# Kernel tuning notes

Hardware: AMD Instinct MI355X
Metric: run time of the kernel (lower is better)

Reference implementation:

```python
import math
import jax
import jax.numpy as jnp
import numpy as np

B = 4096        # number of contexts / segments
T = 262144      # total objects across all segments (avg 64 per segment)
F = 128         # object_size
H = 256         # hidden_size
C = 512         # context_size


def setup_inputs() -> dict:
    key = jax.random.key(0)
    ks = jax.random.split(key, 8)
    objects = jax.random.normal(ks[0], (T, F), dtype=jnp.float32)
    context = jax.random.normal(ks[1], (B, C), dtype=jnp.float32)
    # sorted segment ids; guarantee every segment non-empty by seeding one id per segment
    extra = jax.random.randint(ks[2], (T - B,), 0, B)
    segment_ids = jnp.sort(jnp.concatenate([jnp.arange(B, dtype=extra.dtype), extra])).astype(jnp.int32)
    s = 0.05
    return {
        "objects": objects,
        "context": context,
        "segment_ids": segment_ids,
        "W1": jax.random.normal(ks[3], (F, H), dtype=jnp.float32) * s,
        "b1": jnp.zeros((H,), dtype=jnp.float32),
        "W2": jax.random.normal(ks[4], (H, H), dtype=jnp.float32) * s,
        "b2": jnp.zeros((H,), dtype=jnp.float32),
        "W3": jax.random.normal(ks[5], (H, 2 * H), dtype=jnp.float32) * s,
        "b3": jnp.zeros((2 * H,), dtype=jnp.float32),
        "Wq": jax.random.normal(ks[6], (C, H), dtype=jnp.float32) * s,
        "bq": jnp.zeros((H,), dtype=jnp.float32),
    }


def reference(objects, context, segment_ids, W1, b1, W2, b2, W3, b3, Wq, bq):
    num_segments = context.shape[0]
    # kv MLP: Linear -> ReLU -> Linear -> ReLU -> Linear(2H)
    h = jax.nn.relu(objects @ W1 + b1)
    h = jax.nn.relu(h @ W2 + b2)
    kv = h @ W3 + b3                                   # [T, 2H]
    k, v = jnp.split(kv, 2, axis=1)                    # [T, H] each
    # query per object via repeat_interleave == gather by segment id
    q = (context @ Wq + bq)[segment_ids]               # [T, H]
    logits = jnp.sum(q * k, axis=1) / math.sqrt(k.shape[1])   # [T]
    # per-segment stable softmax
    m = jax.ops.segment_max(logits, segment_ids, num_segments=num_segments)
    e = jnp.exp(logits - m[segment_ids])
    z = jax.ops.segment_sum(e, segment_ids, num_segments=num_segments)
    w = e / z[segment_ids]                             # [T]
    # per-segment weighted sum of values
    embedding = jax.ops.segment_sum(w[:, None] * v, segment_ids, num_segments=num_segments)  # [B, H]
    return embedding, w
```

## Files before the change

### kernel.cpp

```cpp
#include <hip/hip_runtime.h>
#include <hip/hip_bf16.h>

#define T_TOTAL 262144
#define B_SEG   4096

typedef __attribute__((ext_vector_type(8))) short short8;
typedef __attribute__((ext_vector_type(4))) float f32x4;

__device__ __forceinline__ short f2bf(float x) {
    __hip_bfloat16 h = __float2bfloat16(x);
    return *reinterpret_cast<short*>(&h);
}
__device__ __forceinline__ float bf2f(short s) {
    unsigned u = ((unsigned)(unsigned short)s) << 16;
    return __uint_as_float(u);
}

__global__ __launch_bounds__(256) void prep_all(
    const float* __restrict__ W1, const float* __restrict__ W2,
    const float* __restrict__ W3, const float* __restrict__ Wq,
    const float* __restrict__ bq, const float* __restrict__ b3,
    const float* __restrict__ ctx,
    short* __restrict__ W1T, short* __restrict__ W2T, short* __restrict__ W3vT,
    float* __restrict__ bz, float* __restrict__ wc, float* __restrict__ c0,
    float* __restrict__ Wqz, float* __restrict__ cbuf) {
    __shared__ __align__(16) char smem[33280];
    const int b = blockIdx.x, tid = threadIdx.x;

    if (b < 40) {
        float (*t)[68] = reinterpret_cast<float(*)[68]>(smem);
        const float* src; short* dst;
        int k0, n0_src, n0_dst, sstride, dstride;
        if (b < 8) {
            int kt = b >> 2, nt = b & 3;
            src = W1; dst = W1T; sstride = 256; dstride = 128;
            k0 = kt * 64; n0_src = nt * 64; n0_dst = nt * 64;
        } else if (b < 24) {
            int id = b - 8, kt = id >> 2, nt = id & 3;
            src = W2; dst = W2T; sstride = 256; dstride = 256;
            k0 = kt * 64; n0_src = nt * 64; n0_dst = nt * 64;
        } else {
            int id = b - 24, kt = id >> 2, nt = id & 3;
            src = W3; dst = W3vT; sstride = 512; dstride = 256;
            k0 = kt * 64; n0_src = 256 + nt * 64; n0_dst = nt * 64;
        }
        {
            int r = tid >> 4, c4 = (tid & 15) * 4;
#pragma unroll
            for (int p = 0; p < 4; p++) {
                int k = p * 16 + r;
                float4 v = *reinterpret_cast<const float4*>(
                    &src[(size_t)(k0 + k) * sstride + n0_src + c4]);
                *reinterpret_cast<float4*>(&t[k][c4]) = v;
            }
        }
        __syncthreads();
        {
            int n = tid >> 2, kq = tid & 3;
            short8 s0, s1;
#pragma unroll
            for (int i = 0; i < 8; i++) s0[i] = f2bf(t[kq * 16 + i][n]);
#pragma unroll
            for (int i = 0; i < 8; i++) s1[i] = f2bf(t[kq * 16 + 8 + i][n]);
            short* o = &dst[(size_t)(n0_dst + n) * dstride + k0 + kq * 16];
            *reinterpret_cast<short8*>(o) = s0;
            *reinterpret_cast<short8*>(o + 8) = s1;
        }
    } else if (b < 42) {
        if (b == 40) {
            float s = 0.f;
            for (int n = 0; n < 256; n += 4) {
                float4 a = *reinterpret_cast<const float4*>(&W3[(size_t)tid * 512 + n]);
                float4 v = *reinterpret_cast<const float4*>(&bq[n]);
                s += a.x * v.x + a.y * v.y + a.z * v.z + a.w * v.w;
            }
            bz[tid] = s;
        } else {
#pragma unroll
            for (int h = 0; h < 2; h++) {
                int c = h * 256 + tid;
                float s = 0.f;
                for (int n = 0; n < 256; n += 4) {
                    float4 a = *reinterpret_cast<const float4*>(&Wq[(size_t)c * 256 + n]);
                    float4 v = *reinterpret_cast<const float4*>(&b3[n]);
                    s += a.x * v.x + a.y * v.y + a.z * v.z + a.w * v.w;
                }
                wc[c] = s;
            }
            if (tid == 0) {
                float s = 0.f;
                for (int n = 0; n < 256; n++) s += bq[n] * b3[n];
                c0[0] = s;
            }
        }
    } else if (b < 554) {
        float (*wq)[260] = reinterpret_cast<float(*)[260]>(smem);
        float (*w3)[260] = reinterpret_cast<float(*)[260]>(smem + 16640);
        const int id = b - 42;
        const int c0r = (id >> 4) * 16, j0 = (id & 15) * 16;
        {
            int r = tid >> 4, nq = tid & 15;
#pragma unroll
            for (int p = 0; p < 4; p++) {
                int col = nq * 4 + p * 64;
                *reinterpret_cast<float4*>(&wq[r][col]) =
                    *reinterpret_cast<const float4*>(&Wq[(size_t)(c0r + r) * 256 + col]);
                *reinterpret_cast<float4*>(&w3[r][col]) =
                    *reinterpret_cast<const float4*>(&W3[(size_t)(j0 + r) * 512 + col]);
            }
        }
        __syncthreads();
        const int ci = tid >> 4, ji = tid & 15;
        float s = 0.f;
        for (int n = 0; n < 256; n += 4) {
            float4 a = *reinterpret_cast<const float4*>(&wq[ci][n]);
            float4 v = *reinterpret_cast<const float4*>(&w3[ji][n]);
            s += a.x * v.x + a.y * v.y + a.z * v.z + a.w * v.w;
        }
        Wqz[(size_t)(c0r + ci) * 256 + j0 + ji] = s;
    } else {
        const int id = b - 554;
        const int row = id * 32 + (tid >> 3);
        const int l = tid & 7;
        float s = 0.f;
        for (int i = 0; i < 64; i += 4) {
            float4 a = *reinterpret_cast<const float4*>(&ctx[(size_t)row * 512 + l * 64 + i]);
            float4 v = *reinterpret_cast<const float4*>(&wc[l * 64 + i]);
            s += a.x * v.x + a.y * v.y + a.z * v.z + a.w * v.w;
        }
        s += __shfl_xor(s, 1); s += __shfl_xor(s, 2); s += __shfl_xor(s, 4);
        if (l == 0) cbuf[row] = s + c0[0];
    }
}

__global__ __launch_bounds__(256) void zq_kernel(
    const float* __restrict__ ctx, const float* __restrict__ Wqz,
    const float* __restrict__ bz, float* __restrict__ zq) {
    __shared__ float As[2][16][68];
    const int tid = threadIdx.x;
    const int tm = tid & 15, tn = tid >> 4;
    const int row0 = blockIdx.x * 64, col0 = blockIdx.y * 64;
    const int lr = tid >> 2, lk = tid & 3;

    float acc[4][4];
#pragma unroll
    for (int i = 0; i < 4; i++)
#pragma unroll
        for (int j = 0; j < 4; j++) acc[i][j] = 0.f;

    float4 av = *reinterpret_cast<const float4*>(&ctx[(size_t)(row0 + lr) * 512 + lk * 4]);
    for (int c = 0; c < 32; c++) {
        int cur = c & 1;
        As[cur][lk * 4 + 0][lr] = av.x;
        As[cur][lk * 4 + 1][lr] = av.y;
        As[cur][lk * 4 + 2][lr] = av.z;
        As[cur][lk * 4 + 3][lr] = av.w;
        __syncthreads();
        if (c < 31)
            av = *reinterpret_cast<const float4*>(
                &ctx[(size_t)(row0 + lr) * 512 + (c + 1) * 16 + lk * 4]);
#pragma unroll
        for (int k = 0; k < 16; k++) {
            float4 a = *reinterpret_cast<const float4*>(&As[cur][k][tm * 4]);
            float4 b = *reinterpret_cast<const float4*>(
                &Wqz[(size_t)(c * 16 + k) * 256 + col0 + tn * 4]);
#pragma unroll
            for (int i = 0; i < 4; i++) {
                float ai = (i == 0) ? a.x : (i == 1) ? a.y : (i == 2) ? a.z : a.w;
                acc[i][0] += ai * b.x; acc[i][1] += ai * b.y;
                acc[i][2] += ai * b.z; acc[i][3] += ai * b.w;
            }
        }
    }
    float4 bv = *reinterpret_cast<const float4*>(&bz[col0 + tn * 4]);
#pragma unroll
    for (int i = 0; i < 4; i++) {
        float4 o = {acc[i][0] + bv.x, acc[i][1] + bv.y, acc[i][2] + bv.z, acc[i][3] + bv.w};
        *reinterpret_cast<float4*>(&zq[(size_t)(row0 + tm * 4 + i) * 256 + col0 + tn * 4]) = o;
    }
}

template <int K>
__device__ __forceinline__ void run_layer(
    const short* __restrict__ act, const short* __restrict__ Wt,
    int nbase, int l16, int quad, f32x4 acc[4][4]) {
    constexpr int KK = K / 32;
    const f32x4 zero = {0.f, 0.f, 0.f, 0.f};
#pragma unroll
    for (int i = 0; i < 4; i++)
#pragma unroll
        for (int j = 0; j < 4; j++) acc[i][j] = zero;

    int woff[4];
#pragma unroll
    for (int ns = 0; ns < 4; ns++)
        woff[ns] = ((nbase + ns * 16 + l16) * K + quad * 8) * 2;
    const int abase = l16 * K * 2;
    const char* actc = reinterpret_cast<const char*>(act);
    const char* wtc  = reinterpret_cast<const char*>(Wt);

    short8 wbuf[2][4];
    short8 areg[2][4];

    auto loadA = [&](int kk, int slot) {
        const int sg = (((kk * 4 + quad) ^ l16) * 16);
#pragma unroll
        for (int ms = 0; ms < 4; ms++)
            areg[slot][ms] = *reinterpret_cast<const short8*>(
                actc + abase + ms * 16 * K * 2 + sg);
    };
    auto loadW = [&](int kk, int slot) {
#pragma unroll
        for (int ns = 0; ns < 4; ns++)
            wbuf[slot][ns] = *reinterpret_cast<const short8*>(
                wtc + woff[ns] + kk * 64);
    };

    loadW(0, 0); loadA(0, 0);
    loadW(1, 1); loadA(1, 1);
#pragma unroll
    for (int kk = 0; kk < KK; kk++) {
        const int cur = kk & 1;
#pragma unroll
        for (int ms = 0; ms < 4; ms++)
#pragma unroll
            for (int ns = 0; ns < 4; ns++)
                acc[ms][ns] = __builtin_amdgcn_mfma_f32_16x16x32_bf16(
                    wbuf[cur][ns], areg[cur][ms], acc[ms][ns], 0, 0, 0);
        if (kk + 2 < KK) { loadW(kk + 2, cur); loadA(kk + 2, cur); }
    }
}

__global__ __launch_bounds__(256, 3) void mlp_kernel(
    const float* __restrict__ objects, const int* __restrict__ seg_ids,
    const short* __restrict__ W1T, const short* __restrict__ W2T,
    const short* __restrict__ W3vT,
    const float* __restrict__ b1, const float* __restrict__ b2,
    const float* __restrict__ b3,
    const float* __restrict__ zqbuf, const float* __restrict__ cbuf,
    float* __restrict__ logits_out, short* __restrict__ vout) {
    __shared__ __align__(16) short bufH[64 * 256];
    __shared__ float slots[4][64];

    const int tid  = threadIdx.x;
    const int wave = tid >> 6;
    const int lane = tid & 63;
    const int quad = lane >> 4;
    const int l16  = lane & 15;
    const int nbase = wave * 64;
    const int row0  = blockIdx.x * 64;

    {
        const float4* op = reinterpret_cast<const float4*>(objects + (size_t)row0 * 128);
#pragma unroll
        for (int i = 0; i < 4; i++) {
            int u = tid + i * 256;
            int m = u >> 4, kg = u & 15;
            float4 x0 = op[u * 2];
            float4 x1 = op[u * 2 + 1];
            short8 s;
            s[0] = f2bf(x0.x); s[1] = f2bf(x0.y); s[2] = f2bf(x0.z); s[3] = f2bf(x0.w);
            s[4] = f2bf(x1.x); s[5] = f2bf(x1.y); s[6] = f2bf(x1.z); s[7] = f2bf(x1.w);
            *reinterpret_cast<short8*>(&bufH[m * 128 + ((kg ^ (m & 15)) * 8)]) = s;
        }
    }
    __syncthreads();

    f32x4 acc[4][4];

    auto store_act = [&](const float* __restrict__ bias) {
#pragma unroll
        for (int ns = 0; ns < 4; ns++) {
            int n0 = nbase + ns * 16 + quad * 4;
            float4 bv = *reinterpret_cast<const float4*>(&bias[n0]);
#pragma unroll
            for (int ms = 0; ms < 4; ms++) {
                int m = ms * 16 + l16;
                short4 s;
                s.x = f2bf(fmaxf(acc[ms][ns][0] + bv.x, 0.f));
                s.y = f2bf(fmaxf(acc[ms][ns][1] + bv.y, 0.f));
                s.z = f2bf(fmaxf(acc[ms][ns][2] + bv.z, 0.f));
                s.w = f2bf(fmaxf(acc[ms][ns][3] + bv.w, 0.f));
                *reinterpret_cast<short4*>(
                    &bufH[m * 256 + (((n0 >> 3) ^ (m & 15)) * 8) + (n0 & 7)]) = s;
            }
        }
    };

    run_layer<128>(bufH, W1T, nbase, l16, quad, acc);
    __syncthreads();
    store_act(b1);
    __syncthreads();

    run_layer<256>(bufH, W2T, nbase, l16, quad, acc);
    __syncthreads();
    {
        float part[4] = {0.f, 0.f, 0.f, 0.f};
        int segm[4];
#pragma unroll
        for (int ms = 0; ms < 4; ms++) segm[ms] = seg_ids[row0 + ms * 16 + l16];
#pragma unroll
        for (int ns = 0; ns < 4; ns++) {
            int n0 = nbase + ns * 16 + quad * 4;
            float4 bv = *reinterpret_cast<const float4*>(&b2[n0]);
#pragma unroll
            for (int ms = 0; ms < 4; ms++) {
                int m = ms * 16 + l16;
                float h0 = fmaxf(acc[ms][ns][0] + bv.x, 0.f);
                float h1v = fmaxf(acc[ms][ns][1] + bv.y, 0.f);
                float h2v = fmaxf(acc[ms][ns][2] + bv.z, 0.f);
                float h3 = fmaxf(acc[ms][ns][3] + bv.w, 0.f);
                short4 s;
                s.x = f2bf(h0); s.y = f2bf(h1v); s.z = f2bf(h2v); s.w = f2bf(h3);
                *reinterpret_cast<short4*>(
                    &bufH[m * 256 + (((n0 >> 3) ^ (m & 15)) * 8) + (n0 & 7)]) = s;
                float4 zq4 = *reinterpret_cast<const float4*>(
                    &zqbuf[(size_t)segm[ms] * 256 + n0]);
                part[ms] += h0 * zq4.x + h1v * zq4.y + h2v * zq4.z + h3 * zq4.w;
            }
        }
#pragma unroll
        for (int ms = 0; ms < 4; ms++) {
            float p = part[ms];
            p += __shfl_xor(p, 16);
            p += __shfl_xor(p, 32);
            if (quad == 0) slots[wave][ms * 16 + l16] = p;
        }
    }
    __syncthreads();
    if (tid < 64) {
        int seg = seg_ids[row0 + tid];
        float s = slots[0][tid] + slots[1][tid] + slots[2][tid] + slots[3][tid] + cbuf[seg];
        logits_out[row0 + tid] = s * 0.0625f;
    }

    run_layer<256>(bufH, W3vT, nbase, l16, quad, acc);
    __syncthreads();
#pragma unroll
    for (int ns = 0; ns < 4; ns++) {
        int n0 = nbase + ns * 16 + quad * 4;
        float4 bv = *reinterpret_cast<const float4*>(&b3[256 + n0]);
#pragma unroll
        for (int ms = 0; ms < 4; ms++) {
            int m = ms * 16 + l16;
            short4 s;
            s.x = f2bf(acc[ms][ns][0] + bv.x);
            s.y = f2bf(acc[ms][ns][1] + bv.y);
            s.z = f2bf(acc[ms][ns][2] + bv.z);
            s.w = f2bf(acc[ms][ns][3] + bv.w);
            *reinterpret_cast<short4*>(
                &bufH[m * 256 + (((n0 >> 3) ^ (m & 15)) * 8) + (n0 & 7)]) = s;
        }
    }
    __syncthreads();
#pragma unroll
    for (int i = 0; i < 8; i++) {
        int idx = tid + i * 256;
        int m = idx >> 5, sg = idx & 31;
        short8 val = *reinterpret_cast<const short8*>(&bufH[m * 256 + sg * 8]);
        int n0 = (sg ^ (m & 15)) * 8;
        *reinterpret_cast<short8*>(&vout[(size_t)(row0 + m) * 256 + n0]) = val;
    }
}

__global__ __launch_bounds__(256) void seg_starts_kernel(
    const int* __restrict__ seg, int* __restrict__ starts) {
    int t = blockIdx.x * 256 + threadIdx.x;
    if (t >= T_TOTAL) return;
    int s = seg[t];
    if (t == 0) {
        for (int q = 0; q <= s; q++) starts[q] = 0;
    } else {
        int p = seg[t - 1];
        for (int q = p + 1; q <= s; q++) starts[q] = t;
    }
}

__global__ __launch_bounds__(64) void segment_kernel(
    const float* __restrict__ logits, const short* __restrict__ vbuf,
    const int* __restrict__ starts, float* __restrict__ emb,
    float* __restrict__ wout) {
    const int b = blockIdx.x;
    const int lane = threadIdx.x;
    const int start = starts[b];
    const int end = (b == B_SEG - 1) ? T_TOTAL : starts[b + 1];

    float mx = -1e30f;
    for (int t = start + lane; t < end; t += 64) mx = fmaxf(mx, logits[t]);
#pragma unroll
    for (int off = 32; off >= 1; off >>= 1) mx = fmaxf(mx, __shfl_xor(mx, off));

    float s = 0.f;
    for (int t = start + lane; t < end; t += 64) s += __expf(logits[t] - mx);
#pragma unroll
    for (int off = 32; off >= 1; off >>= 1) s += __shfl_xor(s, off);
    const float invz = 1.f / s;

    for (int t = start + lane; t < end; t += 64)
        wout[t] = __expf(logits[t] - mx) * invz;

    float a[4][4];
#pragma unroll
    for (int i = 0; i < 4; i++)
#pragma unroll
        for (int j = 0; j < 4; j++) a[i][j] = 0.f;

    int t = start;
    for (; t + 8 <= end; t += 8) {
#pragma unroll
        for (int u = 0; u < 8; u++) {
            float wv = __expf(logits[t + u] - mx) * invz;
            short4 v4 = *reinterpret_cast<const short4*>(
                &vbuf[(size_t)(t + u) * 256 + lane * 4]);
            a[u & 3][0] += wv * bf2f(v4.x);
            a[u & 3][1] += wv * bf2f(v4.y);
            a[u & 3][2] += wv * bf2f(v4.z);
            a[u & 3][3] += wv * bf2f(v4.w);
        }
    }
    for (; t < end; t++) {
        float wv = __expf(logits[t] - mx) * invz;
        short4 v4 = *reinterpret_cast<const short4*>(
            &vbuf[(size_t)t * 256 + lane * 4]);
        a[0][0] += wv * bf2f(v4.x);
        a[0][1] += wv * bf2f(v4.y);
        a[0][2] += wv * bf2f(v4.z);
        a[0][3] += wv * bf2f(v4.w);
    }
    float4 o;
    o.x = a[0][0] + a[1][0] + a[2][0] + a[3][0];
    o.y = a[0][1] + a[1][1] + a[2][1] + a[3][1];
    o.z = a[0][2] + a[1][2] + a[2][2] + a[3][2];
    o.w = a[0][3] + a[1][3] + a[2][3] + a[3][3];
    *reinterpret_cast<float4*>(&emb[(size_t)b * 256 + lane * 4]) = o;
}

extern "C" void kernel_launch(void* const* d_in, const int* in_sizes, int n_in,
                              void* d_out, int out_size, void* d_ws, size_t ws_size,
                              hipStream_t stream) {
    const float* objects = (const float*)d_in[0];
    const float* context = (const float*)d_in[1];
    const int*   seg     = (const int*)d_in[2];
    const float* W1 = (const float*)d_in[3];
    const float* b1 = (const float*)d_in[4];
    const float* W2 = (const float*)d_in[5];
    const float* b2 = (const float*)d_in[6];
    const float* W3 = (const float*)d_in[7];
    const float* b3 = (const float*)d_in[8];
    const float* Wq = (const float*)d_in[9];
    const float* bq = (const float*)d_in[10];

    char* ws = (char*)d_ws;
    float* zqbuf = (float*)(ws);
    float* cbuf  = (float*)(ws + 4194304);
    int*   seg_starts = (int*)(ws + 4194304);
    short* W1T   = (short*)(ws + 4210688);
    short* W2T   = (short*)(ws + 4276224);
    short* W3vT  = (short*)(ws + 4407296);
    char*  lreg   = ws + 4538368;
    float* logits = (float*)lreg;
    float* Wqz    = (float*)lreg;
    float* bz     = (float*)(lreg + 524288);
    float* wc     = (float*)(lreg + 525312);
    float* c0     = (float*)(lreg + 527360);
    short* vbuf   = (short*)(ws + 5586944);

    float* emb  = (float*)d_out;
    float* wout = emb + (size_t)B_SEG * 256;

    prep_all<<<682, 256, 0, stream>>>(W1, W2, W3, Wq, bq, b3, context,
                                      W1T, W2T, W3vT, bz, wc, c0, Wqz, cbuf);
    zq_kernel<<<dim3(64, 4), 256, 0, stream>>>(context, Wqz, bz, zqbuf);
    mlp_kernel<<<T_TOTAL / 64, 256, 0, stream>>>(objects, seg, W1T, W2T, W3vT,
                                                 b1, b2, b3, zqbuf, cbuf,
                                                 logits, vbuf);
    seg_starts_kernel<<<T_TOTAL / 256, 256, 0, stream>>>(seg, seg_starts);
    segment_kernel<<<B_SEG, 64, 0, stream>>>(logits, vbuf, seg_starts, emb, wout);
}
```

Baseline: 450.9 us.

## Make MLP kernel persistent with prefetched object tiles and fold seg-starts into prep

The MLP kernel becomes a persistent grid of 768 blocks that loops over 64-row tiles. The next tile's objects are prefetched into registers while the current tile computes, so global load latency overlaps with MFMA work. The v output is now written straight from the accumulators instead of being staged through shared memory, and the inner GEMM loop loads A each step with only a single-step W prefetch. The segment-starts computation moves into the prep kernel to drop one launch, which adds register pressure and changes the workspace offsets.

Result: slower. 796.3 us (+76.6%).

```diff
diff --git a/kernel.cpp b/kernel.cpp
--- a/kernel.cpp
+++ b/kernel.cpp
@@ -20,10 +20,11 @@
     const float* __restrict__ W1, const float* __restrict__ W2,
     const float* __restrict__ W3, const float* __restrict__ Wq,
     const float* __restrict__ bq, const float* __restrict__ b3,
-    const float* __restrict__ ctx,
+    const float* __restrict__ ctx, const int* __restrict__ seg,
     short* __restrict__ W1T, short* __restrict__ W2T, short* __restrict__ W3vT,
     float* __restrict__ bz, float* __restrict__ wc, float* __restrict__ c0,
-    float* __restrict__ Wqz, float* __restrict__ cbuf) {
+    float* __restrict__ Wqz, float* __restrict__ cbuf,
+    int* __restrict__ starts) {
     __shared__ __align__(16) char smem[33280];
     const int b = blockIdx.x, tid = threadIdx.x;
 
@@ -118,7 +119,7 @@
             s += a.x * v.x + a.y * v.y + a.z * v.z + a.w * v.w;
         }
         Wqz[(size_t)(c0r + ci) * 256 + j0 + ji] = s;
-    } else {
+    } else if (b < 682) {
         const int id = b - 554;
         const int row = id * 32 + (tid >> 3);
         const int l = tid & 7;
@@ -130,6 +131,17 @@
         }
         s += __shfl_xor(s, 1); s += __shfl_xor(s, 2); s += __shfl_xor(s, 4);
         if (l == 0) cbuf[row] = s + c0[0];
+    } else {
+        int t = (b - 682) * 256 + tid;
+        if (t < T_TOTAL) {
+            int s = seg[t];
+            if (t == 0) {
+                for (int q = 0; q <= s; q++) starts[q] = 0;
+            } else {
+                int p = seg[t - 1];
+                for (int q = p + 1; q <= s; q++) starts[q] = t;
+            }
+        }
     }
 }
 
@@ -200,34 +212,34 @@
     const char* wtc  = reinterpret_cast<const char*>(Wt);
 
     short8 wbuf[2][4];
-    short8 areg[2][4];
-
-    auto loadA = [&](int kk, int slot) {
-        const int sg = (((kk * 4 + quad) ^ l16) * 16);
-#pragma unroll
-        for (int ms = 0; ms < 4; ms++)
-            areg[slot][ms] = *reinterpret_cast<const short8*>(
-                actc + abase + ms * 16 * K * 2 + sg);
-    };
-    auto loadW = [&](int kk, int slot) {
-#pragma unroll
-        for (int ns = 0; ns < 4; ns++)
-            wbuf[slot][ns] = *reinterpret_cast<const short8*>(
-                wtc + woff[ns] + kk * 64);
-    };
-
-    loadW(0, 0); loadA(0, 0);
-    loadW(1, 1); loadA(1, 1);
+    short8 areg[4];
+
+#pragma unroll
+    for (int ns = 0; ns < 4; ns++)
+        wbuf[0][ns] = *reinterpret_cast<const short8*>(wtc + woff[ns]);
+
 #pragma unroll
     for (int kk = 0; kk < KK; kk++) {
-        const int cur = kk & 1;
+        {
+            const int sg = (((kk * 4 + quad) ^ l16) * 16);
+#pragma unroll
+            for (int ms = 0; ms < 4; ms++)
+                areg[ms] = *reinterpret_cast<const short8*>(
+                    actc + abase + ms * 16 * K * 2 + sg);
+        }
+        if (kk + 1 < KK) {
+#pragma unroll
+            for (int ns = 0; ns < 4; ns++)
+                wbuf[(kk + 1) & 1][ns] = *reinterpret_cast<const short8*>(
+                    wtc + woff[ns] + (kk + 1) * 64);
+        }
+        const int cb = kk & 1;
 #pragma unroll
         for (int ms = 0; ms < 4; ms++)
 #pragma unroll
             for (int ns = 0; ns < 4; ns++)
                 acc[ms][ns] = __builtin_amdgcn_mfma_f32_16x16x32_bf16(
-                    wbuf[cur][ns], areg[cur][ms], acc[ms][ns], 0, 0, 0);
-        if (kk + 2 < KK) { loadW(kk + 2, cur); loadA(kk + 2, cur); }
+                    wbuf[cb][ns], areg[ms], acc[ms][ns], 0, 0, 0);
     }
 }
 
@@ -248,23 +260,31 @@
     const int quad = lane >> 4;
     const int l16  = lane & 15;
     const int nbase = wave * 64;
-    const int row0  = blockIdx.x * 64;
-
-    {
-        const float4* op = reinterpret_cast<const float4*>(objects + (size_t)row0 * 128);
+    constexpr int NT = T_TOTAL / 64;
+    const int GRID = gridDim.x;
+
+    float4 xr[8];
+    auto loadX = [&](int t) {
+        const float4* op = reinterpret_cast<const float4*>(objects + (size_t)t * 64 * 128);
+#pragma unroll
+        for (int i = 0; i < 4; i++) {
+            int u = tid + i * 256;
+            xr[2 * i]     = op[u * 2];
+            xr[2 * i + 1] = op[u * 2 + 1];
+        }
+    };
+    auto writeX = [&]() {
 #pragma unroll
         for (int i = 0; i < 4; i++) {
             int u = tid + i * 256;
             int m = u >> 4, kg = u & 15;
-            float4 x0 = op[u * 2];
-            float4 x1 = op[u * 2 + 1];
+            float4 x0 = xr[2 * i], x1 = xr[2 * i + 1];
             short8 s;
             s[0] = f2bf(x0.x); s[1] = f2bf(x0.y); s[2] = f2bf(x0.z); s[3] = f2bf(x0.w);
             s[4] = f2bf(x1.x); s[5] = f2bf(x1.y); s[6] = f2bf(x1.z); s[7] = f2bf(x1.w);
             *reinterpret_cast<short8*>(&bufH[m * 128 + ((kg ^ (m & 15)) * 8)]) = s;
         }
-    }
-    __syncthreads();
+    };
 
     f32x4 acc[4][4];
 
@@ -287,92 +307,81 @@
         }
     };
 
-    run_layer<128>(bufH, W1T, nbase, l16, quad, acc);
-    __syncthreads();
-    store_act(b1);
-    __syncthreads();
-
-    run_layer<256>(bufH, W2T, nbase, l16, quad, acc);
-    __syncthreads();
-    {
-        float part[4] = {0.f, 0.f, 0.f, 0.f};
-        int segm[4];
-#pragma unroll
-        for (int ms = 0; ms < 4; ms++) segm[ms] = seg_ids[row0 + ms * 16 + l16];
+    loadX(blockIdx.x);
+
+    for (int tile = blockIdx.x; tile < NT; tile += GRID) {
+        const int row0 = tile * 64;
+        const int nxt = tile + GRID;
+
+        __syncthreads();
+        writeX();
+        __syncthreads();
+
+        run_layer<128>(bufH, W1T, nbase, l16, quad, acc);
+        __syncthreads();
+        if (nxt < NT) loadX(nxt);
+        store_act(b1);
+        __syncthreads();
+
+        run_layer<256>(bufH, W2T, nbase, l16, quad, acc);
+        __syncthreads();
+        {
+            float part[4] = {0.f, 0.f, 0.f, 0.f};
+            int segm[4];
+#pragma unroll
+            for (int ms = 0; ms < 4; ms++) segm[ms] = seg_ids[row0 + ms * 16 + l16];
+#pragma unroll
+            for (int ns = 0; ns < 4; ns++) {
+                int n0 = nbase + ns * 16 + quad * 4;
+                float4 bv = *reinterpret_cast<const float4*>(&b2[n0]);
+#pragma unroll
+                for (int ms = 0; ms < 4; ms++) {
+                    int m = ms * 16 + l16;
+                    float h0 = fmaxf(acc[ms][ns][0] + bv.x, 0.f);
+                    float h1v = fmaxf(acc[ms][ns][1] + bv.y, 0.f);
+                    float h2v = fmaxf(acc[ms][ns][2] + bv.z, 0.f);
+                    float h3 = fmaxf(acc[ms][ns][3] + bv.w, 0.f);
+                    short4 s;
+                    s.x = f2bf(h0); s.y = f2bf(h1v); s.z = f2bf(h2v); s.w = f2bf(h3);
+                    *reinterpret_cast<short4*>(
+                        &bufH[m * 256 + (((n0 >> 3) ^ (m & 15)) * 8) + (n0 & 7)]) = s;
+                    float4 zq4 = *reinterpret_cast<const float4*>(
+                        &zqbuf[(size_t)segm[ms] * 256 + n0]);
+                    part[ms] += h0 * zq4.x + h1v * zq4.y + h2v * zq4.z + h3 * zq4.w;
+                }
+            }
+#pragma unroll
+            for (int ms = 0; ms < 4; ms++) {
+                float p = part[ms];
+                p += __shfl_xor(p, 16);
+                p += __shfl_xor(p, 32);
+                if (quad == 0) slots[wave][ms * 16 + l16] = p;
+            }
+        }
+        __syncthreads();
+        if (tid < 64) {
+            int seg = seg_ids[row0 + tid];
+            float s = slots[0][tid] + slots[1][tid] + slots[2][tid] + slots[3][tid] + cbuf[seg];
+            logits_out[row0 + tid] = s * 0.0625f;
+        }
+
+        run_layer<256>(bufH, W3vT, nbase, l16, quad, acc);
 #pragma unroll
         for (int ns = 0; ns < 4; ns++) {
             int n0 = nbase + ns * 16 + quad * 4;
-            float4 bv = *reinterpret_cast<const float4*>(&b2[n0]);
+            float4 bv = *reinterpret_cast<const float4*>(&b3[256 + n0]);
 #pragma unroll
             for (int ms = 0; ms < 4; ms++) {
                 int m = ms * 16 + l16;
-                float h0 = fmaxf(acc[ms][ns][0] + bv.x, 0.f);
-                float h1v = fmaxf(acc[ms][ns][1] + bv.y, 0.f);
-                float h2v = fmaxf(acc[ms][ns][2] + bv.z, 0.f);
-                float h3 = fmaxf(acc[ms][ns][3] + bv.w, 0.f);
                 short4 s;
-                s.x = f2bf(h0); s.y = f2bf(h1v); s.z = f2bf(h2v); s.w = f2bf(h3);
+                s.x = f2bf(acc[ms][ns][0] + bv.x);
+                s.y = f2bf(acc[ms][ns][1] + bv.y);
+                s.z = f2bf(acc[ms][ns][2] + bv.z);
+                s.w = f2bf(acc[ms][ns][3] + bv.w);
                 *reinterpret_cast<short4*>(
-                    &bufH[m * 256 + (((n0 >> 3) ^ (m & 15)) * 8) + (n0 & 7)]) = s;
-                float4 zq4 = *reinterpret_cast<const float4*>(
-                    &zqbuf[(size_t)segm[ms] * 256 + n0]);
-                part[ms] += h0 * zq4.x + h1v * zq4.y + h2v * zq4.z + h3 * zq4.w;
-            }
-        }
-#pragma unroll
-        for (int ms = 0; ms < 4; ms++) {
-            float p = part[ms];
-            p += __shfl_xor(p, 16);
-            p += __shfl_xor(p, 32);
-            if (quad == 0) slots[wave][ms * 16 + l16] = p;
-        }
-    }
-    __syncthreads();
-    if (tid < 64) {
-        int seg = seg_ids[row0 + tid];
-        float s = slots[0][tid] + slots[1][tid] + slots[2][tid] + slots[3][tid] + cbuf[seg];
-        logits_out[row0 + tid] = s * 0.0625f;
-    }
-
-    run_layer<256>(bufH, W3vT, nbase, l16, quad, acc);
-    __syncthreads();
-#pragma unroll
-    for (int ns = 0; ns < 4; ns++) {
-        int n0 = nbase + ns * 16 + quad * 4;
-        float4 bv = *reinterpret_cast<const float4*>(&b3[256 + n0]);
-#pragma unroll
-        for (int ms = 0; ms < 4; ms++) {
-            int m = ms * 16 + l16;
-            short4 s;
-            s.x = f2bf(acc[ms][ns][0] + bv.x);
-            s.y = f2bf(acc[ms][ns][1] + bv.y);
-            s.z = f2bf(acc[ms][ns][2] + bv.z);
-            s.w = f2bf(acc[ms][ns][3] + bv.w);
-            *reinterpret_cast<short4*>(
-                &bufH[m * 256 + (((n0 >> 3) ^ (m & 15)) * 8) + (n0 & 7)]) = s;
-        }
-    }
-    __syncthreads();
-#pragma unroll
-    for (int i = 0; i < 8; i++) {
-        int idx = tid + i * 256;
-        int m = idx >> 5, sg = idx & 31;
-        short8 val = *reinterpret_cast<const short8*>(&bufH[m * 256 + sg * 8]);
-        int n0 = (sg ^ (m & 15)) * 8;
-        *reinterpret_cast<short8*>(&vout[(size_t)(row0 + m) * 256 + n0]) = val;
-    }
-}
-
-__global__ __launch_bounds__(256) void seg_starts_kernel(
-    const int* __restrict__ seg, int* __restrict__ starts) {
-    int t = blockIdx.x * 256 + threadIdx.x;
-    if (t >= T_TOTAL) return;
-    int s = seg[t];
-    if (t == 0) {
-        for (int q = 0; q <= s; q++) starts[q] = 0;
-    } else {
-        int p = seg[t - 1];
-        for (int q = p + 1; q <= s; q++) starts[q] = t;
+                    &vout[(size_t)(row0 + m) * 256 + n0]) = s;
+            }
+        }
     }
 }
 
@@ -453,27 +462,27 @@
     char* ws = (char*)d_ws;
     float* zqbuf = (float*)(ws);
     float* cbuf  = (float*)(ws + 4194304);
-    int*   seg_starts = (int*)(ws + 4194304);
-    short* W1T   = (short*)(ws + 4210688);
-    short* W2T   = (short*)(ws + 4276224);
-    short* W3vT  = (short*)(ws + 4407296);
-    char*  lreg   = ws + 4538368;
+    int*   seg_starts = (int*)(ws + 4227072);
+    short* W1T   = (short*)(ws + 4259840);
+    short* W2T   = (short*)(ws + 4325376);
+    short* W3vT  = (short*)(ws + 4456448);
+    char*  lreg   = ws + 4587520;
     float* logits = (float*)lreg;
     float* Wqz    = (float*)lreg;
     float* bz     = (float*)(lreg + 524288);
     float* wc     = (float*)(lreg + 525312);
     float* c0     = (float*)(lreg + 527360);
-    short* vbuf   = (short*)(ws + 5586944);
+    short* vbuf   = (short*)(ws + 5636096);
 
     float* emb  = (float*)d_out;
     float* wout = emb + (size_t)B_SEG * 256;
 
-    prep_all<<<682, 256, 0, stream>>>(W1, W2, W3, Wq, bq, b3, context,
-                                      W1T, W2T, W3vT, bz, wc, c0, Wqz, cbuf);
+    prep_all<<<1706, 256, 0, stream>>>(W1, W2, W3, Wq, bq, b3, context, seg,
+                                       W1T, W2T, W3vT, bz, wc, c0, Wqz, cbuf,
+                                       seg_starts);
     zq_kernel<<<dim3(64, 4), 256, 0, stream>>>(context, Wqz, bz, zqbuf);
-    mlp_kernel<<<T_TOTAL / 64, 256, 0, stream>>>(objects, seg, W1T, W2T, W3vT,
-                                                 b1, b2, b3, zqbuf, cbuf,
-                                                 logits, vbuf);
-    seg_starts_kernel<<<T_TOTAL / 256, 256, 0, stream>>>(seg, seg_starts);
+    mlp_kernel<<<768, 256, 0, stream>>>(objects, seg, W1T, W2T, W3vT,
+                                        b1, b2, b3, zqbuf, cbuf,
+                                        logits, vbuf);
     segment_kernel<<<B_SEG, 64, 0, stream>>>(logits, vbuf, seg_starts, emb, wout);
 }
```
